# Kernel tuning notes

Measured on AMD Instinct MI355X. Metric: run time of the kernel, lower is better.

Reference implementation:

```python
import jax, jax.numpy as jnp
import numpy as np

TEMPERATURE = 8.0  # sqrt(d_k) with d_k=64
NEG = -9e15        # matches torch zero_vec constant -9000000000000000.0


def setup_inputs() -> dict:
    key = jax.random.key(0)
    k1, k2, k3, k4 = jax.random.split(key, 4)
    a, b, N, d = 32, 4, 1024, 64  # a = nhead*b, nhead = 8
    q = jax.random.normal(k1, (a, N, d), dtype=jnp.float32)
    k = jax.random.normal(k2, (a, N, d), dtype=jnp.float32)
    v = jax.random.normal(k3, (a, N, d), dtype=jnp.float32)
    adj = jax.random.randint(k4, (b, N, N), 0, 2, dtype=jnp.int32)
    return {"q": q, "k": k, "v": v, "adj": adj}


def reference(q, k, v, adj):
    # q,k,v: [nhead*b, N, d]; adj: [b, N, N]
    a, N, d = v.shape
    b = adj.shape[0]
    nhead = a // b
    # scores: [a, N, N]
    attn = jnp.einsum('bnd,bmd->bnm', q, k) / jnp.asarray(TEMPERATURE, q.dtype)
    # 'local' focus: mask by adjacency, broadcast over heads (head-major layout
    # matches torch's adj.unsqueeze(0).repeat(nhead,1,1,1).view(-1,N,N))
    attn = attn.reshape(nhead, b, N, N)
    attn = jnp.where(adj[None] > 0, attn, jnp.asarray(NEG, attn.dtype))
    attn = attn.reshape(a, N, N)
    attn = jax.nn.softmax(attn, axis=2)
    # dropout p=0.0 -> identity
    output = jnp.einsum('bnm,bmd->bnd', attn, v)
    return (output, attn)
```

## Files before the change

kernel.cpp:

```cpp
#include <hip/hip_runtime.h>
#include <hip/hip_bf16.h>

#define A_TOT 32
#define SEQ 1024
#define DIM 64
#define NT 16
#define GSTRIDE 1056
#define TILEB (8 * GSTRIDE)

typedef __attribute__((ext_vector_type(8))) short short8;
typedef __attribute__((ext_vector_type(4))) float f32x4;
typedef unsigned long long u64;

static __device__ __forceinline__ unsigned pack2bf(float a, float b) {
    union { __hip_bfloat16 h[2]; unsigned u; } x;
    x.h[0] = __float2bfloat16(a);
    x.h[1] = __float2bfloat16(b);
    return x.u;
}

static __device__ __forceinline__ void gload_lds16(const void* g, void* l) {
    __builtin_amdgcn_global_load_lds(
        (const __attribute__((address_space(1))) unsigned*)g,
        (__attribute__((address_space(3))) unsigned*)l, 16, 0, 0);
}

static __device__ __forceinline__ short8 lds_frag(const unsigned char* tile,
                                                  int row, int chunk) {
    const int byte = (row >> 3) * GSTRIDE + (row & 7) * 128 +
                     ((chunk ^ (row & 7)) << 4);
    return *reinterpret_cast<const short8*>(tile + byte);
}

#define WAITBAR(N) do {                                          \
    asm volatile("s_waitcnt vmcnt(" #N ")" ::: "memory");        \
    __builtin_amdgcn_sched_barrier(0);                           \
    __builtin_amdgcn_s_barrier();                                \
    __builtin_amdgcn_sched_barrier(0);                           \
    asm volatile("" ::: "memory");                               \
} while (0)

__global__ void prepass_kernel(const float* __restrict__ q,
                               const float* __restrict__ k,
                               const float* __restrict__ v,
                               const int* __restrict__ adj,
                               __hip_bfloat16* __restrict__ qb,
                               __hip_bfloat16* __restrict__ kb,
                               __hip_bfloat16* __restrict__ vt,
                               u64* __restrict__ adjm) {
    __shared__ __hip_bfloat16 tile[64][65];
    const int tid = threadIdx.x;
    if (blockIdx.y < 2) {
        const float* src = blockIdx.y ? k : q;
        __hip_bfloat16* dst = blockIdx.y ? kb : qb;
        int i = (blockIdx.x * 256 + tid) * 4;
        float4 f = *reinterpret_cast<const float4*>(src + i);
        union { __hip_bfloat16 h[4]; ushort4 u; } cv;
        cv.h[0] = __float2bfloat16(f.x);
        cv.h[1] = __float2bfloat16(f.y);
        cv.h[2] = __float2bfloat16(f.z);
        cv.h[3] = __float2bfloat16(f.w);
        *reinterpret_cast<ushort4*>(dst + i) = cv.u;
        return;
    }
    if (blockIdx.x < 512) {
        const int bh = blockIdx.x >> 4;
        const int n0 = (blockIdx.x & 15) * 64;
        const float* vsrc = v + ((size_t)bh * SEQ + n0) * DIM;
        for (int e = tid; e < 64 * 64; e += 256) {
            int i = e >> 6;
            int d = e & 63;
            tile[i][d] = __float2bfloat16(vsrc[(size_t)i * DIM + d]);
        }
        __syncthreads();
        __hip_bfloat16* vdst = vt + (size_t)bh * DIM * SEQ + n0;
        for (int e = tid; e < 64 * 64; e += 256) {
            int d = e >> 6;
            int i = e & 63;
            vdst[(size_t)d * SEQ + i] = tile[i][d];
        }
        return;
    }
    if (blockIdx.x < 1536) {
        const int px   = blockIdx.x - 512;
        const int wv   = tid >> 6;
        const int lane = tid & 63;
        const int wbase = px * 64 + wv * 16;
        for (int it = 0; it < 16; ++it) {
            const int w = wbase + it;
            const int a = adj[(size_t)w * 64 + lane];
            u64 m = __ballot(a > 0);
            if (lane == 0) adjm[w] = m;
        }
    }
}

__launch_bounds__(256)
__global__ void graph_attn_kernel(const __hip_bfloat16* __restrict__ qb,
                                  const __hip_bfloat16* __restrict__ kb,
                                  const __hip_bfloat16* __restrict__ vt,
                                  const u64* __restrict__ adjm,
                                  float* __restrict__ out,
                                  float* __restrict__ attn) {
    __shared__ __align__(16) unsigned char kstage[3][TILEB];
    __shared__ __align__(16) unsigned char vstage[3][TILEB];
    __shared__ float part[4][4][16];
    __shared__ float lsum_sh[4][16];

    const int wg    = (blockIdx.x & 7) * 64 + (blockIdx.x >> 3);
    const int bh    = wg >> 4;
    const int rb    = wg & 15;
    const int batch = bh & 3;
    const int tid   = threadIdx.x;
    const int wid   = tid >> 6;
    const int lane  = tid & 63;
    const int lr    = lane & 15;
    const int lgi   = lane >> 4;
    const int row16 = rb * 64 + wid * 16;

    const int sub  = lane >> 3;
    const int csrc = (lane & 7) ^ sub;

    const __hip_bfloat16* qrow = qb + ((size_t)bh * SEQ + row16 + lr) * DIM + lgi * 8;
    const short8 qf0 = *reinterpret_cast<const short8*>(qrow);
    const short8 qf1 = *reinterpret_cast<const short8*>(qrow + 32);

    const u64* mrow = adjm + ((size_t)batch * SEQ + row16 + lr) * (SEQ / 64);
    const __hip_bfloat16* kbh = kb + (size_t)bh * SEQ * DIM;
    const __hip_bfloat16* vth = vt + (size_t)bh * DIM * SEQ;

    const int kperm = (lr >> 2) * 8 + (lr & 3);

    auto stageK = [&](int t, int b) {
        const __hip_bfloat16* g0 = kbh + (size_t)(t * 64 + wid * 16) * DIM;
        unsigned char* l0 = &kstage[b][(wid * 2) * GSTRIDE];
        gload_lds16(g0 + (size_t)sub * DIM + csrc * 8, l0);
        gload_lds16(g0 + (size_t)(8 + sub) * DIM + csrc * 8, l0 + GSTRIDE);
    };
    auto stageV = [&](int t, int b) {
        const __hip_bfloat16* g0 = vth + (size_t)(wid * 16) * SEQ + t * 64;
        unsigned char* l0 = &vstage[b][(wid * 2) * GSTRIDE];
        gload_lds16(g0 + (size_t)sub * SEQ + csrc * 8, l0);
        gload_lds16(g0 + (size_t)(8 + sub) * SEQ + csrc * 8, l0 + GSTRIDE);
    };

    u64 mb = mrow[0], mn_ = 0;
    stageK(0, 0);
    stageK(1, 1);
    WAITBAR(2);

    float lp = 0.f;
    int cur = 0;
    for (int t = 0; t < NT; ++t) {
        if (t < NT - 1) mn_ = mrow[t + 1];
        if (t < NT - 2) {
            int b2 = cur + 2; if (b2 >= 3) b2 -= 3;
            stageK(t + 2, b2);
        }
#pragma unroll
        for (int c = 0; c < 4; ++c) {
            const int cb = (c >> 1) * 32 + (c & 1) * 4;
            const int krow = cb + kperm;
            short8 kf0 = lds_frag(kstage[cur], krow, lgi);
            short8 kf1 = lds_frag(kstage[cur], krow, 4 + lgi);
            f32x4 acc = {0.f, 0.f, 0.f, 0.f};
            acc = __builtin_amdgcn_mfma_f32_16x16x32_bf16(kf0, qf0, acc, 0, 0, 0);
            acc = __builtin_amdgcn_mfma_f32_16x16x32_bf16(kf1, qf1, acc, 0, 0, 0);
            const unsigned b4 = (unsigned)(mb >> (cb + lgi * 8)) & 0xFu;
            float p0 = (b4 & 1u) ? __expf(acc[0] * 0.125f) : 0.f;
            float p1 = (b4 & 2u) ? __expf(acc[1] * 0.125f) : 0.f;
            float p2 = (b4 & 4u) ? __expf(acc[2] * 0.125f) : 0.f;
            float p3 = (b4 & 8u) ? __expf(acc[3] * 0.125f) : 0.f;
            lp += (p0 + p1) + (p2 + p3);
        }
        if (t < NT - 1) {
            mb = mn_;
            WAITBAR(2);
        }
        ++cur; if (cur >= 3) cur -= 3;
    }

    part[wid][lgi][lr] = lp;
    asm volatile("" ::: "memory");
    if (lane < 16) {
        lsum_sh[wid][lane] = part[wid][0][lane] + part[wid][1][lane] +
                             part[wid][2][lane] + part[wid][3][lane];
    }
    __syncthreads();
    const float linv = 1.0f / (lsum_sh[wid][lr] + 1e-37f);

    f32x4 o[4];
#pragma unroll
    for (int c = 0; c < 4; ++c) o[c] = (f32x4){0.f, 0.f, 0.f, 0.f};

    mb = mrow[0];
    stageK(0, 0); stageV(0, 0);
    stageK(1, 1); stageV(1, 1);
    WAITBAR(4);

    float* attn_row = attn + (size_t)bh * SEQ * SEQ + (size_t)(row16 + lr) * SEQ;
    unsigned pk[4][2];
    cur = 0;
    for (int t = 0; t < NT; ++t) {
        if (t > 0) {
            const int tp = t - 1;
#pragma unroll
            for (int c = 0; c < 4; ++c) {
                const int cb = (c >> 1) * 32 + (c & 1) * 4;
                const unsigned u01 = pk[c][0];
                const unsigned u23 = pk[c][1];
                float f0 = __uint_as_float(u01 << 16);
                float f1 = __uint_as_float(u01 & 0xffff0000u);
                float f2 = __uint_as_float(u23 << 16);
                float f3 = __uint_as_float(u23 & 0xffff0000u);
                *reinterpret_cast<float4*>(attn_row + tp * 64 + cb + lgi * 8) =
                    (float4){f0, f1, f2, f3};
            }
        }
        if (t < NT - 1) mn_ = mrow[t + 1];
        if (t < NT - 2) {
            int b2 = cur + 2; if (b2 >= 3) b2 -= 3;
            stageK(t + 2, b2);
            stageV(t + 2, b2);
        }
#pragma unroll
        for (int c = 0; c < 4; ++c) {
            const int cb = (c >> 1) * 32 + (c & 1) * 4;
            const int krow = cb + kperm;
            short8 kf0 = lds_frag(kstage[cur], krow, lgi);
            short8 kf1 = lds_frag(kstage[cur], krow, 4 + lgi);
            f32x4 acc = {0.f, 0.f, 0.f, 0.f};
            acc = __builtin_amdgcn_mfma_f32_16x16x32_bf16(kf0, qf0, acc, 0, 0, 0);
            acc = __builtin_amdgcn_mfma_f32_16x16x32_bf16(kf1, qf1, acc, 0, 0, 0);
            const unsigned b4 = (unsigned)(mb >> (cb + lgi * 8)) & 0xFu;
            float p0 = (b4 & 1u) ? __expf(acc[0] * 0.125f) * linv : 0.f;
            float p1 = (b4 & 2u) ? __expf(acc[1] * 0.125f) * linv : 0.f;
            float p2 = (b4 & 4u) ? __expf(acc[2] * 0.125f) * linv : 0.f;
            float p3 = (b4 & 8u) ? __expf(acc[3] * 0.125f) * linv : 0.f;
            pk[c][0] = pack2bf(p0, p1);
            pk[c][1] = pack2bf(p2, p3);
        }
        union { unsigned u[4]; short8 s; } pf0, pf1;
        pf0.u[0] = pk[0][0]; pf0.u[1] = pk[0][1];
        pf0.u[2] = pk[1][0]; pf0.u[3] = pk[1][1];
        pf1.u[0] = pk[2][0]; pf1.u[1] = pk[2][1];
        pf1.u[2] = pk[3][0]; pf1.u[3] = pk[3][1];
#pragma unroll
        for (int c2 = 0; c2 < 4; ++c2) {
            const int vrow = c2 * 16 + lr;
            short8 vf0 = lds_frag(vstage[cur], vrow, lgi);
            short8 vf1 = lds_frag(vstage[cur], vrow, 4 + lgi);
            o[c2] = __builtin_amdgcn_mfma_f32_16x16x32_bf16(pf0.s, vf0, o[c2], 0, 0, 0);
            o[c2] = __builtin_amdgcn_mfma_f32_16x16x32_bf16(pf1.s, vf1, o[c2], 0, 0, 0);
        }
        if (t < NT - 1) {
            mb = mn_;
            WAITBAR(4);
        }
        ++cur; if (cur >= 3) cur -= 3;
    }

#pragma unroll
    for (int c = 0; c < 4; ++c) {
        const int cb = (c >> 1) * 32 + (c & 1) * 4;
        const unsigned u01 = pk[c][0];
        const unsigned u23 = pk[c][1];
        float f0 = __uint_as_float(u01 << 16);
        float f1 = __uint_as_float(u01 & 0xffff0000u);
        float f2 = __uint_as_float(u23 << 16);
        float f3 = __uint_as_float(u23 & 0xffff0000u);
        *reinterpret_cast<float4*>(attn_row + (NT - 1) * 64 + cb + lgi * 8) =
            (float4){f0, f1, f2, f3};
    }

    float* ob = out + (size_t)bh * SEQ * DIM + (size_t)row16 * DIM;
#pragma unroll
    for (int c2 = 0; c2 < 4; ++c2)
#pragma unroll
        for (int j = 0; j < 4; ++j)
            ob[(size_t)(lgi * 4 + j) * DIM + c2 * 16 + lr] = o[c2][j];
}

extern "C" void kernel_launch(void* const* d_in, const int* in_sizes, int n_in,
                              void* d_out, int out_size, void* d_ws, size_t ws_size,
                              hipStream_t stream) {
    const float* q   = (const float*)d_in[0];
    const float* k   = (const float*)d_in[1];
    const float* v   = (const float*)d_in[2];
    const int*   adj = (const int*)d_in[3];

    float* out  = (float*)d_out;
    float* attn = out + (size_t)A_TOT * SEQ * DIM;

    __hip_bfloat16* qb = (__hip_bfloat16*)d_ws;
    __hip_bfloat16* kb = qb + (size_t)A_TOT * SEQ * DIM;
    __hip_bfloat16* vt = kb + (size_t)A_TOT * SEQ * DIM;
    u64* adjm = (u64*)(vt + (size_t)A_TOT * SEQ * DIM);

    prepass_kernel<<<dim3(2048, 3), 256, 0, stream>>>(q, k, v, adj, qb, kb, vt, adjm);
    graph_attn_kernel<<<512, 256, 0, stream>>>(qb, kb, vt, adjm, out, attn);
}
```

Measured before the change: 64.00 us.

## Merge two-pass softmax into single pass with deferred normalization

Fuses the row-sum pass and the P·V pass into one sweep over K/V tiles. Unnormalized exp values are packed to bf16 and kept in registers for every tile (128 registers per lane), and the output and attention rows are scaled by the inverse row sum at the end. This drops the second QK^T computation and the second exponentiation, but raises register pressure heavily, which may lower occupancy or cause spills. It also delays all attention stores to after the loop, and since there is no max subtraction, large scores could overflow the bf16 exp values.

```diff
diff --git a/kernel.cpp b/kernel.cpp
--- a/kernel.cpp
+++ b/kernel.cpp
@@ -145,17 +145,24 @@
     };
 
     u64 mb = mrow[0], mn_ = 0;
-    stageK(0, 0);
-    stageK(1, 1);
-    WAITBAR(2);
+    stageK(0, 0); stageV(0, 0);
+    stageK(1, 1); stageV(1, 1);
+    WAITBAR(4);
 
     float lp = 0.f;
+    unsigned p_pk[NT][4][2];
+    f32x4 o[4];
+#pragma unroll
+    for (int c = 0; c < 4; ++c) o[c] = (f32x4){0.f, 0.f, 0.f, 0.f};
+
     int cur = 0;
+#pragma unroll
     for (int t = 0; t < NT; ++t) {
         if (t < NT - 1) mn_ = mrow[t + 1];
         if (t < NT - 2) {
             int b2 = cur + 2; if (b2 >= 3) b2 -= 3;
             stageK(t + 2, b2);
+            stageV(t + 2, b2);
         }
 #pragma unroll
         for (int c = 0; c < 4; ++c) {
@@ -172,79 +179,14 @@
             float p2 = (b4 & 4u) ? __expf(acc[2] * 0.125f) : 0.f;
             float p3 = (b4 & 8u) ? __expf(acc[3] * 0.125f) : 0.f;
             lp += (p0 + p1) + (p2 + p3);
-        }
-        if (t < NT - 1) {
-            mb = mn_;
-            WAITBAR(2);
-        }
-        ++cur; if (cur >= 3) cur -= 3;
-    }
-
-    part[wid][lgi][lr] = lp;
-    asm volatile("" ::: "memory");
-    if (lane < 16) {
-        lsum_sh[wid][lane] = part[wid][0][lane] + part[wid][1][lane] +
-                             part[wid][2][lane] + part[wid][3][lane];
-    }
-    __syncthreads();
-    const float linv = 1.0f / (lsum_sh[wid][lr] + 1e-37f);
-
-    f32x4 o[4];
-#pragma unroll
-    for (int c = 0; c < 4; ++c) o[c] = (f32x4){0.f, 0.f, 0.f, 0.f};
-
-    mb = mrow[0];
-    stageK(0, 0); stageV(0, 0);
-    stageK(1, 1); stageV(1, 1);
-    WAITBAR(4);
-
-    float* attn_row = attn + (size_t)bh * SEQ * SEQ + (size_t)(row16 + lr) * SEQ;
-    unsigned pk[4][2];
-    cur = 0;
-    for (int t = 0; t < NT; ++t) {
-        if (t > 0) {
-            const int tp = t - 1;
-#pragma unroll
-            for (int c = 0; c < 4; ++c) {
-                const int cb = (c >> 1) * 32 + (c & 1) * 4;
-                const unsigned u01 = pk[c][0];
-                const unsigned u23 = pk[c][1];
-                float f0 = __uint_as_float(u01 << 16);
-                float f1 = __uint_as_float(u01 & 0xffff0000u);
-                float f2 = __uint_as_float(u23 << 16);
-                float f3 = __uint_as_float(u23 & 0xffff0000u);
-                *reinterpret_cast<float4*>(attn_row + tp * 64 + cb + lgi * 8) =
-                    (float4){f0, f1, f2, f3};
-            }
-        }
-        if (t < NT - 1) mn_ = mrow[t + 1];
-        if (t < NT - 2) {
-            int b2 = cur + 2; if (b2 >= 3) b2 -= 3;
-            stageK(t + 2, b2);
-            stageV(t + 2, b2);
-        }
-#pragma unroll
-        for (int c = 0; c < 4; ++c) {
-            const int cb = (c >> 1) * 32 + (c & 1) * 4;
-            const int krow = cb + kperm;
-            short8 kf0 = lds_frag(kstage[cur], krow, lgi);
-            short8 kf1 = lds_frag(kstage[cur], krow, 4 + lgi);
-            f32x4 acc = {0.f, 0.f, 0.f, 0.f};
-            acc = __builtin_amdgcn_mfma_f32_16x16x32_bf16(kf0, qf0, acc, 0, 0, 0);
-            acc = __builtin_amdgcn_mfma_f32_16x16x32_bf16(kf1, qf1, acc, 0, 0, 0);
-            const unsigned b4 = (unsigned)(mb >> (cb + lgi * 8)) & 0xFu;
-            float p0 = (b4 & 1u) ? __expf(acc[0] * 0.125f) * linv : 0.f;
-            float p1 = (b4 & 2u) ? __expf(acc[1] * 0.125f) * linv : 0.f;
-            float p2 = (b4 & 4u) ? __expf(acc[2] * 0.125f) * linv : 0.f;
-            float p3 = (b4 & 8u) ? __expf(acc[3] * 0.125f) * linv : 0.f;
-            pk[c][0] = pack2bf(p0, p1);
-            pk[c][1] = pack2bf(p2, p3);
+            p_pk[t][c][0] = pack2bf(p0, p1);
+            p_pk[t][c][1] = pack2bf(p2, p3);
         }
         union { unsigned u[4]; short8 s; } pf0, pf1;
-        pf0.u[0] = pk[0][0]; pf0.u[1] = pk[0][1];
-        pf0.u[2] = pk[1][0]; pf0.u[3] = pk[1][1];
-        pf1.u[0] = pk[2][0]; pf1.u[1] = pk[2][1];
-        pf1.u[2] = pk[3][0]; pf1.u[3] = pk[3][1];
+        pf0.u[0] = p_pk[t][0][0]; pf0.u[1] = p_pk[t][0][1];
+        pf0.u[2] = p_pk[t][1][0]; pf0.u[3] = p_pk[t][1][1];
+        pf1.u[0] = p_pk[t][2][0]; pf1.u[1] = p_pk[t][2][1];
+        pf1.u[2] = p_pk[t][3][0]; pf1.u[3] = p_pk[t][3][1];
 #pragma unroll
         for (int c2 = 0; c2 < 4; ++c2) {
             const int vrow = c2 * 16 + lr;
@@ -255,22 +197,40 @@
         }
         if (t < NT - 1) {
             mb = mn_;
-            WAITBAR(4);
+            if (t < NT - 2) WAITBAR(4); else WAITBAR(0);
         }
         ++cur; if (cur >= 3) cur -= 3;
     }
 
-#pragma unroll
-    for (int c = 0; c < 4; ++c) {
-        const int cb = (c >> 1) * 32 + (c & 1) * 4;
-        const unsigned u01 = pk[c][0];
-        const unsigned u23 = pk[c][1];
-        float f0 = __uint_as_float(u01 << 16);
-        float f1 = __uint_as_float(u01 & 0xffff0000u);
-        float f2 = __uint_as_float(u23 << 16);
-        float f3 = __uint_as_float(u23 & 0xffff0000u);
-        *reinterpret_cast<float4*>(attn_row + (NT - 1) * 64 + cb + lgi * 8) =
-            (float4){f0, f1, f2, f3};
+    part[wid][lgi][lr] = lp;
+    asm volatile("" ::: "memory");
+    if (lane < 16) {
+        lsum_sh[wid][lane] = part[wid][0][lane] + part[wid][1][lane] +
+                             part[wid][2][lane] + part[wid][3][lane];
+    }
+    __syncthreads();
+
+    const float linv_r = 1.0f / (lsum_sh[wid][lr] + 1e-37f);
+    float ltot[4];
+#pragma unroll
+    for (int j = 0; j < 4; ++j)
+        ltot[j] = 1.0f / (lsum_sh[wid][lgi * 4 + j] + 1e-37f);
+
+    float* attn_row = attn + (size_t)bh * SEQ * SEQ + (size_t)(row16 + lr) * SEQ;
+#pragma unroll
+    for (int t = 0; t < NT; ++t) {
+#pragma unroll
+        for (int c = 0; c < 4; ++c) {
+            const int cb = (c >> 1) * 32 + (c & 1) * 4;
+            const unsigned u01 = p_pk[t][c][0];
+            const unsigned u23 = p_pk[t][c][1];
+            float f0 = __uint_as_float(u01 << 16) * linv_r;
+            float f1 = __uint_as_float(u01 & 0xffff0000u) * linv_r;
+            float f2 = __uint_as_float(u23 << 16) * linv_r;
+            float f3 = __uint_as_float(u23 & 0xffff0000u) * linv_r;
+            *reinterpret_cast<float4*>(attn_row + t * 64 + cb + lgi * 8) =
+                (float4){f0, f1, f2, f3};
+        }
     }
 
     float* ob = out + (size_t)bh * SEQ * DIM + (size_t)row16 * DIM;
@@ -278,7 +238,7 @@
     for (int c2 = 0; c2 < 4; ++c2)
 #pragma unroll
         for (int j = 0; j < 4; ++j)
-            ob[(size_t)(lgi * 4 + j) * DIM + c2 * 16 + lr] = o[c2][j];
+            ob[(size_t)(lgi * 4 + j) * DIM + c2 * 16 + lr] = o[c2][j] * ltot[j];
 }
 
 extern "C" void kernel_launch(void* const* d_in, const int* in_sizes, int n_in,
```

Result: slower. 70.66 us (+10.4%).

## Switch K/V staging to double buffering and store attn tiles immediately

Applied to the files above, without the earlier changes.

Reduces the K and V LDS staging rings from three buffers to two, prefetching one tile ahead instead of two, and adjusts the wait counts to match. The attention-probability stores move from being deferred to the next iteration to being issued right after each tile is computed. This removes the epilogue store loop. The smaller LDS footprint may allow more workgroups per CU. The cost is a shallower prefetch, so load latency is less hidden, and the WAITBAR(4) count now relies on the stores sitting behind the loads in the vmcnt queue.

```diff
diff --git a/kernel.cpp b/kernel.cpp
--- a/kernel.cpp
+++ b/kernel.cpp
@@ -102,8 +102,8 @@
                                   const u64* __restrict__ adjm,
                                   float* __restrict__ out,
                                   float* __restrict__ attn) {
-    __shared__ __align__(16) unsigned char kstage[3][TILEB];
-    __shared__ __align__(16) unsigned char vstage[3][TILEB];
+    __shared__ __align__(16) unsigned char kstage[2][TILEB];
+    __shared__ __align__(16) unsigned char vstage[2][TILEB];
     __shared__ float part[4][4][16];
     __shared__ float lsum_sh[4][16];
 
@@ -146,16 +146,14 @@
 
     u64 mb = mrow[0], mn_ = 0;
     stageK(0, 0);
-    stageK(1, 1);
-    WAITBAR(2);
+    WAITBAR(0);
 
     float lp = 0.f;
     int cur = 0;
     for (int t = 0; t < NT; ++t) {
-        if (t < NT - 1) mn_ = mrow[t + 1];
-        if (t < NT - 2) {
-            int b2 = cur + 2; if (b2 >= 3) b2 -= 3;
-            stageK(t + 2, b2);
+        if (t < NT - 1) {
+            mn_ = mrow[t + 1];
+            stageK(t + 1, cur ^ 1);
         }
 #pragma unroll
         for (int c = 0; c < 4; ++c) {
@@ -175,9 +173,9 @@
         }
         if (t < NT - 1) {
             mb = mn_;
-            WAITBAR(2);
-        }
-        ++cur; if (cur >= 3) cur -= 3;
+            WAITBAR(0);
+        }
+        cur ^= 1;
     }
 
     part[wid][lgi][lr] = lp;
@@ -195,33 +193,16 @@
 
     mb = mrow[0];
     stageK(0, 0); stageV(0, 0);
-    stageK(1, 1); stageV(1, 1);
-    WAITBAR(4);
+    WAITBAR(0);
 
     float* attn_row = attn + (size_t)bh * SEQ * SEQ + (size_t)(row16 + lr) * SEQ;
     unsigned pk[4][2];
     cur = 0;
     for (int t = 0; t < NT; ++t) {
-        if (t > 0) {
-            const int tp = t - 1;
-#pragma unroll
-            for (int c = 0; c < 4; ++c) {
-                const int cb = (c >> 1) * 32 + (c & 1) * 4;
-                const unsigned u01 = pk[c][0];
-                const unsigned u23 = pk[c][1];
-                float f0 = __uint_as_float(u01 << 16);
-                float f1 = __uint_as_float(u01 & 0xffff0000u);
-                float f2 = __uint_as_float(u23 << 16);
-                float f3 = __uint_as_float(u23 & 0xffff0000u);
-                *reinterpret_cast<float4*>(attn_row + tp * 64 + cb + lgi * 8) =
-                    (float4){f0, f1, f2, f3};
-            }
-        }
-        if (t < NT - 1) mn_ = mrow[t + 1];
-        if (t < NT - 2) {
-            int b2 = cur + 2; if (b2 >= 3) b2 -= 3;
-            stageK(t + 2, b2);
-            stageV(t + 2, b2);
+        if (t < NT - 1) {
+            mn_ = mrow[t + 1];
+            stageK(t + 1, cur ^ 1);
+            stageV(t + 1, cur ^ 1);
         }
 #pragma unroll
         for (int c = 0; c < 4; ++c) {
@@ -240,6 +221,18 @@
             pk[c][0] = pack2bf(p0, p1);
             pk[c][1] = pack2bf(p2, p3);
         }
+#pragma unroll
+        for (int c = 0; c < 4; ++c) {
+            const int cb = (c >> 1) * 32 + (c & 1) * 4;
+            const unsigned u01 = pk[c][0];
+            const unsigned u23 = pk[c][1];
+            float f0 = __uint_as_float(u01 << 16);
+            float f1 = __uint_as_float(u01 & 0xffff0000u);
+            float f2 = __uint_as_float(u23 << 16);
+            float f3 = __uint_as_float(u23 & 0xffff0000u);
+            *reinterpret_cast<float4*>(attn_row + t * 64 + cb + lgi * 8) =
+                (float4){f0, f1, f2, f3};
+        }
         union { unsigned u[4]; short8 s; } pf0, pf1;
         pf0.u[0] = pk[0][0]; pf0.u[1] = pk[0][1];
         pf0.u[2] = pk[1][0]; pf0.u[3] = pk[1][1];
@@ -257,20 +250,7 @@
             mb = mn_;
             WAITBAR(4);
         }
-        ++cur; if (cur >= 3) cur -= 3;
-    }
-
-#pragma unroll
-    for (int c = 0; c < 4; ++c) {
-        const int cb = (c >> 1) * 32 + (c & 1) * 4;
-        const unsigned u01 = pk[c][0];
-        const unsigned u23 = pk[c][1];
-        float f0 = __uint_as_float(u01 << 16);
-        float f1 = __uint_as_float(u01 & 0xffff0000u);
-        float f2 = __uint_as_float(u23 << 16);
-        float f3 = __uint_as_float(u23 & 0xffff0000u);
-        *reinterpret_cast<float4*>(attn_row + (NT - 1) * 64 + cb + lgi * 8) =
-            (float4){f0, f1, f2, f3};
+        cur ^= 1;
     }
 
     float* ob = out + (size_t)bh * SEQ * DIM + (size_t)row16 * DIM;
```

After: 61.87 us, median of 2. 3.3% less time.
